# Kernel tuning notes

Measured on AMD Instinct MI355X. Metric: run time of the kernel, lower is better.

## Reference

```python
import jax, jax.numpy as jnp
import numpy as np

B, S, D, H, T = 64, 512, 1024, 1024, 9


def setup_inputs() -> dict:
    key = jax.random.key(0)
    ks = jax.random.split(key, 8)
    return {
        "input_": jax.random.normal(ks[0], (B, S, D), dtype=jnp.float32),
        "labels": jax.random.randint(ks[1], (B, S), 0, T),
        "attention_mask": jnp.ones((B, S), dtype=jnp.int32),
        # linear_1: input_dim -> hidden_dim (stored [in, out])
        "W1": (jax.random.normal(ks[2], (D, H), dtype=jnp.float32) * 0.02),
        "b1": jnp.zeros((H,), dtype=jnp.float32),
        # linear_2: hidden_dim -> tag_dim
        "W2": (jax.random.normal(ks[3], (H, T), dtype=jnp.float32) * 0.02),
        "b2": jnp.zeros((T,), dtype=jnp.float32),
        # torchcrf params: uniform(-0.1, 0.1)
        "start_trans": jax.random.uniform(ks[4], (T,), minval=-0.1, maxval=0.1),
        "end_trans": jax.random.uniform(ks[5], (T,), minval=-0.1, maxval=0.1),
        "trans": jax.random.uniform(ks[6], (T, T), minval=-0.1, maxval=0.1),
    }


def _crf_mean_llh(logits, tags, mask, start, end, trans):
    """torchcrf.CRF log-likelihood, reduction='mean'. logits [B,S,T]."""
    nb = logits.shape[0]
    em = jnp.transpose(logits, (1, 0, 2))          # [S,B,T] time-major
    tg = tags.T                                    # [S,B]
    m = mask.T.astype(logits.dtype)                # [S,B]
    bidx = jnp.arange(nb)

    # --- numerator: score of the gold path ---
    score0 = start[tg[0]] + em[0, bidx, tg[0]]

    def num_step(carry, x):
        score, last = carry
        em_t, tag_t, m_t = x
        score = score + (trans[last, tag_t] + em_t[bidx, tag_t]) * m_t
        last = jnp.where(m_t > 0, tag_t, last)
        return (score, last), None

    (score, last), _ = jax.lax.scan(num_step, (score0, tg[0]), (em[1:], tg[1:], m[1:]))
    score = score + end[last]

    # --- denominator: log-partition via logsumexp forward recurrence ---
    alpha0 = start[None, :] + em[0]                # [B,T]

    def part_step(alpha, x):
        em_t, m_t = x
        # [B, prev T, next T] semiring (log-sum-exp) matrix product
        nxt = jax.nn.logsumexp(alpha[:, :, None] + trans[None, :, :] + em_t[:, None, :], axis=1)
        alpha = jnp.where(m_t[:, None] > 0, nxt, alpha)
        return alpha, None

    alpha, _ = jax.lax.scan(part_step, alpha0, (em[1:], m[1:]))
    log_z = jax.nn.logsumexp(alpha + end[None, :], axis=1)

    return jnp.mean(score - log_z)


def reference(input_, labels, attention_mask, W1, b1, W2, b2, start_trans, end_trans, trans):
    # dropout layers are identity in eval mode
    h = input_ @ W1 + b1                           # [B,S,H]
    logits = h @ W2 + b2                           # [B,S,T]
    llh = _crf_mean_llh(logits, labels, attention_mask, start_trans, end_trans, trans)
    loss = -llh                                    # forward returns (-1*crf_llh, logits)
    return (loss, logits)
```

## Files before the change

### kernel.cpp

```cpp
#include <hip/hip_runtime.h>

#define BD 64
#define SD 512
#define DD 1024
#define HD 1024
#define TD 9
#define NSEG 8
#define SEGL 64
#define NEGI -1e30f

__device__ __forceinline__ float lse9(const float v[9]) {
    float m0 = fmaxf(v[0], v[1]);
    float m1 = fmaxf(v[2], v[3]);
    float m2 = fmaxf(v[4], v[5]);
    float m3 = fmaxf(v[6], v[7]);
    float mx = fmaxf(fmaxf(m0, m1), fmaxf(fmaxf(m2, m3), v[8]));
    float s = __expf(v[0] - mx) + __expf(v[1] - mx) + __expf(v[2] - mx)
            + __expf(v[3] - mx) + __expf(v[4] - mx) + __expf(v[5] - mx)
            + __expf(v[6] - mx) + __expf(v[7] - mx) + __expf(v[8] - mx);
    return mx + __logf(s);
}

__global__ __launch_bounds__(256) void k_w12(const float* __restrict__ W1,
                                             const float* __restrict__ b1,
                                             const float* __restrict__ W2,
                                             const float* __restrict__ b2,
                                             float* __restrict__ W12t,
                                             float* __restrict__ b12) {
    __shared__ float sh_w2[HD * TD];
    __shared__ float wred[4][TD];
    const int tid = threadIdx.x;
    const int wave = tid >> 6, lane = tid & 63;
    const int d = blockIdx.x;

    for (int i = tid; i < HD * TD / 4; i += 256)
        ((float4*)sh_w2)[i] = ((const float4*)W2)[i];
    __syncthreads();

    const float* row = (d < DD) ? (W1 + (size_t)d * HD) : b1;
    float4 x = ((const float4*)row)[tid];

    float acc[TD];
#pragma unroll
    for (int t = 0; t < TD; t++) acc[t] = 0.f;
#pragma unroll
    for (int u = 0; u < 4; u++) {
        float xv = (&x.x)[u];
        int h = tid * 4 + u;
#pragma unroll
        for (int t = 0; t < TD; t++) acc[t] += xv * sh_w2[h * TD + t];
    }
#pragma unroll
    for (int t = 0; t < TD; t++) {
        float v = acc[t];
#pragma unroll
        for (int m = 1; m < 64; m <<= 1) v += __shfl_xor(v, m);
        acc[t] = v;
    }
    if (lane == 0) {
#pragma unroll
        for (int t = 0; t < TD; t++) wred[wave][t] = acc[t];
    }
    __syncthreads();
    if (tid < TD) {
        float s = wred[0][tid] + wred[1][tid] + wred[2][tid] + wred[3][tid];
        if (d < DD) W12t[tid * DD + d] = s;
        else        b12[tid] = s + b2[tid];
    }
}

__global__ __launch_bounds__(256) void k_gemm2(const float* __restrict__ X,
                                               const float* __restrict__ W12t,
                                               const float* __restrict__ b12,
                                               float* __restrict__ logits) {
    __shared__ float wt[TD][DD];
    __shared__ float bb[TD];

    for (int i = threadIdx.x; i < TD * DD / 4; i += 256)
        ((float4*)&wt[0][0])[i] = ((const float4*)W12t)[i];
    if (threadIdx.x < TD) bb[threadIdx.x] = b12[threadIdx.x];
    __syncthreads();

    const int wave = threadIdx.x >> 6;
    const int lane = threadIdx.x & 63;
    const int g = lane >> 4;
    const int l16 = lane & 15;
    const int row0 = blockIdx.x * 32 + wave * 8 + g * 2;

    const float4* xr0 = (const float4*)(X + (size_t)row0 * DD);
    const float4* xr1 = xr0 + DD / 4;

    float acc0[TD], acc1[TD];
#pragma unroll
    for (int t = 0; t < TD; t++) { acc0[t] = 0.f; acc1[t] = 0.f; }

#pragma unroll 4
    for (int k = 0; k < 16; k++) {
        int d4 = l16 + k * 16;
        float4 x0 = xr0[d4];
        float4 x1 = xr1[d4];
#pragma unroll
        for (int t = 0; t < TD; t++) {
            const float4 w = *(const float4*)&wt[t][d4 * 4];
            acc0[t] += x0.x * w.x + x0.y * w.y + x0.z * w.z + x0.w * w.w;
            acc1[t] += x1.x * w.x + x1.y * w.y + x1.z * w.z + x1.w * w.w;
        }
    }

#pragma unroll
    for (int t = 0; t < TD; t++) {
        float v0 = acc0[t], v1 = acc1[t];
        v0 += __shfl_xor(v0, 1); v1 += __shfl_xor(v1, 1);
        v0 += __shfl_xor(v0, 2); v1 += __shfl_xor(v1, 2);
        v0 += __shfl_xor(v0, 4); v1 += __shfl_xor(v1, 4);
        v0 += __shfl_xor(v0, 8); v1 += __shfl_xor(v1, 8);
        acc0[t] = v0; acc1[t] = v1;
    }

    float* out0 = logits + (size_t)row0 * TD;
    float* out1 = out0 + TD;
    if (l16 < TD) {
        out0[l16] = acc0[l16] + bb[l16];
        out1[l16] = acc1[l16] + bb[l16];
    }
}

__global__ __launch_bounds__(256) void k_crf_seg(const float* __restrict__ logits,
                                                 const int* __restrict__ maskp,
                                                 const float* __restrict__ transp,
                                                 float* __restrict__ segP) {
    const int blk = blockIdx.x;
    const int b = blk >> 3, s = blk & 7;
    const int tid = threadIdx.x;

    __shared__ float tr[81];
    __shared__ float em[SEGL * 9];
    __shared__ int   mk[SEGL];
    __shared__ float bufA[32 * 81];
    __shared__ float bufB[16 * 81];

    const int t0 = s * SEGL + 1;

    for (int i = tid; i < SEGL * 9; i += 256) {
        int q = i / 9, j = i - q * 9;
        int t = t0 + q;
        em[i] = (t < SD) ? logits[((size_t)b * SD + t) * TD + j] : 0.f;
    }
    if (tid < SEGL) {
        int t = t0 + tid;
        mk[tid] = (t < SD) ? maskp[b * SD + t] : 0;
    }
    if (tid < 81) tr[tid] = transp[tid];
    __syncthreads();

    for (int e = tid; e < 32 * 81; e += 256) {
        int p = e / 81, r = e - p * 81;
        int i = r / 9, j = r - i * 9;
        int la = 2 * p, lb = 2 * p + 1;
        int mA = mk[la], mB = mk[lb];
        float out;
        if (mA && mB) {
            float v[9];
#pragma unroll
            for (int k = 0; k < 9; k++)
                v[k] = tr[i * 9 + k] + em[la * 9 + k] + tr[k * 9 + j];
            out = lse9(v) + em[lb * 9 + j];
        } else if (mA) {
            out = tr[r] + em[la * 9 + j];
        } else if (mB) {
            out = tr[r] + em[lb * 9 + j];
        } else {
            out = (i == j) ? 0.f : NEGI;
        }
        bufA[e] = out;
    }
    __syncthreads();

#define COMBINE(SRC, DST, NP)                                        \
    for (int e = tid; e < (NP) * 81; e += 256) {                     \
        int p = e / 81, r = e - p * 81;                              \
        int i = r / 9, j = r - i * 9;                                \
        const float* Am = (SRC) + (2 * p) * 81;                      \
        const float* Bm = (SRC) + (2 * p + 1) * 81;                  \
        float v[9];                                                  \
        _Pragma("unroll")                                            \
        for (int k = 0; k < 9; k++) v[k] = Am[i * 9 + k] + Bm[k * 9 + j]; \
        (DST)[e] = lse9(v);                                          \
    }                                                                \
    __syncthreads();

    COMBINE(bufA, bufB, 16)
    COMBINE(bufB, bufA, 8)
    COMBINE(bufA, bufB, 4)
    COMBINE(bufB, bufA, 2)

    if (tid < 81) {
        int i = tid / 9, j = tid - (tid / 9) * 9;
        float v[9];
#pragma unroll
        for (int k = 0; k < 9; k++) v[k] = bufA[i * 9 + k] + bufA[81 + k * 9 + j];
        segP[(size_t)blk * 81 + tid] = lse9(v);
    }
}

__global__ __launch_bounds__(256) void k_crf_fin(const float* __restrict__ logits,
                                                 const int* __restrict__ labels,
                                                 const int* __restrict__ maskp,
                                                 const float* __restrict__ startp,
                                                 const float* __restrict__ endp,
                                                 const float* __restrict__ transp,
                                                 const float* __restrict__ segP,
                                                 float* __restrict__ diff) {
    const int b = blockIdx.x;
    const int tid = threadIdx.x;

    __shared__ float S[8 * 81];
    __shared__ float A4[4 * 81];
    __shared__ float A2[2 * 81];
    __shared__ float P[81];
    __shared__ float finv[81];
    __shared__ float red[256];
    __shared__ int   redi[256];

    for (int i = tid; i < 8 * 81; i += 256) S[i] = segP[(size_t)b * 8 * 81 + i];
    __syncthreads();

    for (int e = tid; e < 4 * 81; e += 256) {
        int p = e / 81, r = e - p * 81;
        int i = r / 9, j = r - i * 9;
        const float* Am = S + (2 * p) * 81;
        const float* Bm = S + (2 * p + 1) * 81;
        float v[9];
#pragma unroll
        for (int k = 0; k < 9; k++) v[k] = Am[i * 9 + k] + Bm[k * 9 + j];
        A4[e] = lse9(v);
    }
    __syncthreads();

    for (int e = tid; e < 2 * 81; e += 256) {
        int p = e / 81, r = e - p * 81;
        int i = r / 9, j = r - i * 9;
        const float* Am = A4 + (2 * p) * 81;
        const float* Bm = A4 + (2 * p + 1) * 81;
        float v[9];
#pragma unroll
        for (int k = 0; k < 9; k++) v[k] = Am[i * 9 + k] + Bm[k * 9 + j];
        A2[e] = lse9(v);
    }
    __syncthreads();

    if (tid < 81) {
        int i = tid / 9, j = tid - (tid / 9) * 9;
        float v[9];
#pragma unroll
        for (int k = 0; k < 9; k++) v[k] = A2[i * 9 + k] + A2[81 + k * 9 + j];
        P[tid] = lse9(v);
    }
    __syncthreads();

    if (tid < 81) {
        int k = tid / 9, j = tid - (tid / 9) * 9;
        finv[tid] = startp[k] + logits[(size_t)b * SD * TD + k] + P[tid] + endp[j];
    }

    float part = 0.f;
    for (int t = 1 + tid; t < SD; t += 256) {
        if (maskp[b * SD + t]) {
            int tgp = labels[b * SD + t - 1];
            int tgc = labels[b * SD + t];
            part += transp[tgp * TD + tgc] + logits[((size_t)b * SD + t) * TD + tgc];
        }
    }
    int lastt = 0;
    for (int t = tid; t < SD; t += 256) {
        if (maskp[b * SD + t]) lastt = max(lastt, t);
    }
    red[tid] = part;
    redi[tid] = lastt;
    __syncthreads();

    if (tid < 64) {
        float p4 = red[tid] + red[tid + 64] + red[tid + 128] + red[tid + 192];
        int l4 = max(max(redi[tid], redi[tid + 64]), max(redi[tid + 128], redi[tid + 192]));
#pragma unroll
        for (int m = 1; m < 64; m <<= 1) {
            p4 += __shfl_xor(p4, m);
            l4 = max(l4, __shfl_xor(l4, m));
        }
        float v1 = finv[tid];
        float v2 = (tid + 64 < 81) ? finv[tid + 64] : NEGI;
        float mx = fmaxf(v1, v2);
#pragma unroll
        for (int m = 1; m < 64; m <<= 1) mx = fmaxf(mx, __shfl_xor(mx, m));
        float ssum = __expf(v1 - mx) + __expf(v2 - mx);
#pragma unroll
        for (int m = 1; m < 64; m <<= 1) ssum += __shfl_xor(ssum, m);
        float logz = mx + __logf(ssum);

        if (tid == 0) {
            int tg0 = labels[b * SD];
            int tgl = labels[b * SD + l4];
            float score = p4 + startp[tg0] + logits[(size_t)b * SD * TD + tg0] + endp[tgl];
            diff[b] = score - logz;
        }
    }
}

__global__ __launch_bounds__(64) void k_loss(const float* __restrict__ diff,
                                             float* __restrict__ out) {
    float v = (threadIdx.x < BD) ? diff[threadIdx.x] : 0.f;
#pragma unroll
    for (int m = 1; m < 64; m <<= 1) v += __shfl_xor(v, m);
    if (threadIdx.x == 0) out[0] = -v / (float)BD;
}

extern "C" void kernel_launch(void* const* d_in, const int* in_sizes, int n_in,
                              void* d_out, int out_size, void* d_ws, size_t ws_size,
                              hipStream_t stream) {
    const float* X      = (const float*)d_in[0];
    const int*   labels = (const int*)d_in[1];
    const int*   maskp  = (const int*)d_in[2];
    const float* W1     = (const float*)d_in[3];
    const float* b1     = (const float*)d_in[4];
    const float* W2     = (const float*)d_in[5];
    const float* b2     = (const float*)d_in[6];
    const float* startp = (const float*)d_in[7];
    const float* endp   = (const float*)d_in[8];
    const float* transp = (const float*)d_in[9];

    float* out = (float*)d_out;
    float* ws = (float*)d_ws;

    float* diff = ws;
    float* W12t = ws + 64;
    float* b12  = ws + 64 + DD * TD;
    float* segP = ws + 64 + DD * TD + 16;
    float* logits = out + 1;

    hipLaunchKernelGGL(k_w12, dim3(DD + 1), dim3(256), 0, stream,
                       W1, b1, W2, b2, W12t, b12);
    hipLaunchKernelGGL(k_gemm2, dim3(BD * SD / 32), dim3(256), 0, stream,
                       X, W12t, b12, logits);
    hipLaunchKernelGGL(k_crf_seg, dim3(BD * NSEG), dim3(256), 0, stream,
                       logits, maskp, transp, segP);
    hipLaunchKernelGGL(k_crf_fin, dim3(BD), dim3(256), 0, stream,
                       logits, labels, maskp, startp, endp, transp, segP, diff);
    hipLaunchKernelGGL(k_loss, dim3(1), dim3(64), 0, stream, diff, out);
}
```

Before: 60.32 us.

## Fuse CRF segment, final, and loss kernels via atomic last-block election

Merges the CRF segment reduction, per-batch finalisation and loss reduction into one kernel. The last segment block of each batch, chosen with an atomic counter, does the per-batch combine, and the last batch does the mean loss. The counters are reset in the first kernel. The log-semiring matrix combines are also restructured so each thread computes a whole row of 9 outputs, reusing the loaded A row. This removes two kernel launches and their serialization, at the cost of tail work on a few elected blocks and lower per-stage thread parallelism.

```diff
diff --git a/kernel.cpp b/kernel.cpp
--- a/kernel.cpp
+++ b/kernel.cpp
@@ -26,12 +26,15 @@
                                              const float* __restrict__ W2,
                                              const float* __restrict__ b2,
                                              float* __restrict__ W12t,
-                                             float* __restrict__ b12) {
+                                             float* __restrict__ b12,
+                                             unsigned int* __restrict__ cnt) {
     __shared__ float sh_w2[HD * TD];
     __shared__ float wred[4][TD];
     const int tid = threadIdx.x;
     const int wave = tid >> 6, lane = tid & 63;
     const int d = blockIdx.x;
+
+    if (blockIdx.x == 0 && tid < 80) cnt[tid] = 0u;
 
     for (int i = tid; i < HD * TD / 4; i += 256)
         ((float4*)sh_w2)[i] = ((const float4*)W2)[i];
@@ -125,10 +128,16 @@
     }
 }
 
-__global__ __launch_bounds__(256) void k_crf_seg(const float* __restrict__ logits,
+__global__ __launch_bounds__(256) void k_crf_all(const float* __restrict__ logits,
+                                                 const int* __restrict__ labels,
                                                  const int* __restrict__ maskp,
+                                                 const float* __restrict__ startp,
+                                                 const float* __restrict__ endp,
                                                  const float* __restrict__ transp,
-                                                 float* __restrict__ segP) {
+                                                 float* __restrict__ segP,
+                                                 float* __restrict__ diff,
+                                                 unsigned int* __restrict__ cnt,
+                                                 float* __restrict__ out) {
     const int blk = blockIdx.x;
     const int b = blk >> 3, s = blk & 7;
     const int tid = threadIdx.x;
@@ -138,6 +147,7 @@
     __shared__ int   mk[SEGL];
     __shared__ float bufA[32 * 81];
     __shared__ float bufB[16 * 81];
+    __shared__ int   elect1, elect2;
 
     const int t0 = s * SEGL + 1;
 
@@ -153,116 +163,91 @@
     if (tid < 81) tr[tid] = transp[tid];
     __syncthreads();
 
-    for (int e = tid; e < 32 * 81; e += 256) {
-        int p = e / 81, r = e - p * 81;
-        int i = r / 9, j = r - i * 9;
+    for (int task = tid; task < 32 * 9; task += 256) {
+        int p = task / 9, i = task - p * 9;
         int la = 2 * p, lb = 2 * p + 1;
         int mA = mk[la], mB = mk[lb];
-        float out;
+        float tri[9];
+#pragma unroll
+        for (int k = 0; k < 9; k++) tri[k] = tr[i * 9 + k];
+        float* dst = bufA + p * 81 + i * 9;
         if (mA && mB) {
-            float v[9];
-#pragma unroll
-            for (int k = 0; k < 9; k++)
-                v[k] = tr[i * 9 + k] + em[la * 9 + k] + tr[k * 9 + j];
-            out = lse9(v) + em[lb * 9 + j];
+            float pre[9];
+#pragma unroll
+            for (int k = 0; k < 9; k++) pre[k] = tri[k] + em[la * 9 + k];
+            for (int j = 0; j < 9; j++) {
+                float v[9];
+#pragma unroll
+                for (int k = 0; k < 9; k++) v[k] = pre[k] + tr[k * 9 + j];
+                dst[j] = lse9(v) + em[lb * 9 + j];
+            }
         } else if (mA) {
-            out = tr[r] + em[la * 9 + j];
+#pragma unroll
+            for (int j = 0; j < 9; j++) dst[j] = tri[j] + em[la * 9 + j];
         } else if (mB) {
-            out = tr[r] + em[lb * 9 + j];
+#pragma unroll
+            for (int j = 0; j < 9; j++) dst[j] = tri[j] + em[lb * 9 + j];
         } else {
-            out = (i == j) ? 0.f : NEGI;
-        }
-        bufA[e] = out;
-    }
-    __syncthreads();
-
-#define COMBINE(SRC, DST, NP)                                        \
-    for (int e = tid; e < (NP) * 81; e += 256) {                     \
-        int p = e / 81, r = e - p * 81;                              \
-        int i = r / 9, j = r - i * 9;                                \
-        const float* Am = (SRC) + (2 * p) * 81;                      \
-        const float* Bm = (SRC) + (2 * p + 1) * 81;                  \
-        float v[9];                                                  \
-        _Pragma("unroll")                                            \
-        for (int k = 0; k < 9; k++) v[k] = Am[i * 9 + k] + Bm[k * 9 + j]; \
-        (DST)[e] = lse9(v);                                          \
-    }                                                                \
+#pragma unroll
+            for (int j = 0; j < 9; j++) dst[j] = (i == j) ? 0.f : NEGI;
+        }
+    }
+    __syncthreads();
+
+#define COMBINE(SRC, DST, NP)                                          \
+    for (int task = tid; task < (NP) * 9; task += 256) {               \
+        int p = task / 9, i = task - p * 9;                            \
+        const float* Am = (SRC) + (2 * p) * 81;                        \
+        const float* Bm = (SRC) + (2 * p + 1) * 81;                    \
+        float ar[9];                                                   \
+        _Pragma("unroll")                                              \
+        for (int k = 0; k < 9; k++) ar[k] = Am[i * 9 + k];             \
+        float* dst = (DST) + p * 81 + i * 9;                           \
+        for (int j = 0; j < 9; j++) {                                  \
+            float v[9];                                                \
+            _Pragma("unroll")                                          \
+            for (int k = 0; k < 9; k++) v[k] = ar[k] + Bm[k * 9 + j];  \
+            dst[j] = lse9(v);                                          \
+        }                                                              \
+    }                                                                  \
     __syncthreads();
 
     COMBINE(bufA, bufB, 16)
     COMBINE(bufB, bufA, 8)
     COMBINE(bufA, bufB, 4)
     COMBINE(bufB, bufA, 2)
-
-    if (tid < 81) {
-        int i = tid / 9, j = tid - (tid / 9) * 9;
-        float v[9];
-#pragma unroll
-        for (int k = 0; k < 9; k++) v[k] = bufA[i * 9 + k] + bufA[81 + k * 9 + j];
-        segP[(size_t)blk * 81 + tid] = lse9(v);
-    }
-}
-
-__global__ __launch_bounds__(256) void k_crf_fin(const float* __restrict__ logits,
-                                                 const int* __restrict__ labels,
-                                                 const int* __restrict__ maskp,
-                                                 const float* __restrict__ startp,
-                                                 const float* __restrict__ endp,
-                                                 const float* __restrict__ transp,
-                                                 const float* __restrict__ segP,
-                                                 float* __restrict__ diff) {
-    const int b = blockIdx.x;
-    const int tid = threadIdx.x;
-
-    __shared__ float S[8 * 81];
-    __shared__ float A4[4 * 81];
-    __shared__ float A2[2 * 81];
-    __shared__ float P[81];
-    __shared__ float finv[81];
-    __shared__ float red[256];
-    __shared__ int   redi[256];
-
-    for (int i = tid; i < 8 * 81; i += 256) S[i] = segP[(size_t)b * 8 * 81 + i];
-    __syncthreads();
-
-    for (int e = tid; e < 4 * 81; e += 256) {
-        int p = e / 81, r = e - p * 81;
-        int i = r / 9, j = r - i * 9;
-        const float* Am = S + (2 * p) * 81;
-        const float* Bm = S + (2 * p + 1) * 81;
-        float v[9];
-#pragma unroll
-        for (int k = 0; k < 9; k++) v[k] = Am[i * 9 + k] + Bm[k * 9 + j];
-        A4[e] = lse9(v);
-    }
-    __syncthreads();
-
-    for (int e = tid; e < 2 * 81; e += 256) {
-        int p = e / 81, r = e - p * 81;
-        int i = r / 9, j = r - i * 9;
-        const float* Am = A4 + (2 * p) * 81;
-        const float* Bm = A4 + (2 * p + 1) * 81;
-        float v[9];
-#pragma unroll
-        for (int k = 0; k < 9; k++) v[k] = Am[i * 9 + k] + Bm[k * 9 + j];
-        A2[e] = lse9(v);
-    }
-    __syncthreads();
-
-    if (tid < 81) {
-        int i = tid / 9, j = tid - (tid / 9) * 9;
-        float v[9];
-#pragma unroll
-        for (int k = 0; k < 9; k++) v[k] = A2[i * 9 + k] + A2[81 + k * 9 + j];
-        P[tid] = lse9(v);
-    }
-    __syncthreads();
-
+    COMBINE(bufA, bufB, 1)
+
+    if (tid < 81) segP[(size_t)blk * 81 + tid] = bufB[tid];
+    __syncthreads();
+
+    if (tid == 0) {
+        __threadfence();
+        unsigned int old = __hip_atomic_fetch_add(&cnt[b], 1u, __ATOMIC_ACQ_REL,
+                                                  __HIP_MEMORY_SCOPE_AGENT);
+        elect1 = (old == NSEG - 1);
+    }
+    __syncthreads();
+    if (!elect1) return;
+
+    for (int i = tid; i < 8 * 81; i += 256)
+        bufA[i] = __hip_atomic_load(&segP[(size_t)b * 8 * 81 + i], __ATOMIC_RELAXED,
+                                    __HIP_MEMORY_SCOPE_AGENT);
+    __syncthreads();
+
+    COMBINE(bufA, bufB, 4)
+    COMBINE(bufB, bufA + 648, 2)
+    COMBINE(bufA + 648, bufB + 324, 1)
+
+    const float* P = bufB + 324;
+    float* finv = bufA + 1600;
     if (tid < 81) {
         int k = tid / 9, j = tid - (tid / 9) * 9;
         finv[tid] = startp[k] + logits[(size_t)b * SD * TD + k] + P[tid] + endp[j];
     }
 
+    float* red = bufA + 900;
+    int* redi = (int*)(bufA + 1200);
     float part = 0.f;
     for (int t = 1 + tid; t < SD; t += 256) {
         if (maskp[b * SD + t]) {
@@ -304,14 +289,24 @@
             diff[b] = score - logz;
         }
     }
-}
-
-__global__ __launch_bounds__(64) void k_loss(const float* __restrict__ diff,
-                                             float* __restrict__ out) {
-    float v = (threadIdx.x < BD) ? diff[threadIdx.x] : 0.f;
-#pragma unroll
-    for (int m = 1; m < 64; m <<= 1) v += __shfl_xor(v, m);
-    if (threadIdx.x == 0) out[0] = -v / (float)BD;
+    __syncthreads();
+
+    if (tid == 0) {
+        __threadfence();
+        unsigned int old = __hip_atomic_fetch_add(&cnt[64], 1u, __ATOMIC_ACQ_REL,
+                                                  __HIP_MEMORY_SCOPE_AGENT);
+        elect2 = (old == BD - 1);
+    }
+    __syncthreads();
+    if (!elect2) return;
+
+    if (tid < 64) {
+        float v = __hip_atomic_load(&diff[tid], __ATOMIC_RELAXED,
+                                    __HIP_MEMORY_SCOPE_AGENT);
+#pragma unroll
+        for (int m = 1; m < 64; m <<= 1) v += __shfl_xor(v, m);
+        if (tid == 0) out[0] = -v / (float)BD;
+    }
 }
 
 extern "C" void kernel_launch(void* const* d_in, const int* in_sizes, int n_in,
@@ -335,15 +330,13 @@
     float* W12t = ws + 64;
     float* b12  = ws + 64 + DD * TD;
     float* segP = ws + 64 + DD * TD + 16;
+    unsigned int* cnt = (unsigned int*)(ws + 64 + DD * TD + 16 + BD * NSEG * 81);
     float* logits = out + 1;
 
     hipLaunchKernelGGL(k_w12, dim3(DD + 1), dim3(256), 0, stream,
-                       W1, b1, W2, b2, W12t, b12);
+                       W1, b1, W2, b2, W12t, b12, cnt);
     hipLaunchKernelGGL(k_gemm2, dim3(BD * SD / 32), dim3(256), 0, stream,
                        X, W12t, b12, logits);
-    hipLaunchKernelGGL(k_crf_seg, dim3(BD * NSEG), dim3(256), 0, stream,
-                       logits, maskp, transp, segP);
-    hipLaunchKernelGGL(k_crf_fin, dim3(BD), dim3(256), 0, stream,
-                       logits, labels, maskp, startp, endp, transp, segP, diff);
-    hipLaunchKernelGGL(k_loss, dim3(1), dim3(64), 0, stream, diff, out);
-}
+    hipLaunchKernelGGL(k_crf_all, dim3(BD * NSEG), dim3(256), 0, stream,
+                       logits, labels, maskp, startp, endp, transp, segP, diff, cnt, out);
+}
```

After: 82.32 us. +36.5%, slower.
